# Kernel tuning notes

Measured on AMD Instinct MI355X. Metric: run time of the kernel, lower is better.

## Reference

```python
import jax, jax.numpy as jnp
import numpy as np

N_EXPERTS = 8
TOP_K = 2


def setup_inputs() -> dict:
    key = jax.random.key(0)
    k1, k2, k3, k4 = jax.random.split(key, 4)
    B, S, D, E = 8, 4096, 1024, N_EXPERTS
    x = jax.random.normal(k1, (B, S, D), dtype=jnp.float32)
    gate_w = jax.random.normal(k2, (D, E), dtype=jnp.float32) * (1.0 / np.sqrt(D))
    expert_w = jax.random.normal(k3, (E, D, D), dtype=jnp.float32) * (1.0 / np.sqrt(D))
    expert_b = jax.random.normal(k4, (E, D), dtype=jnp.float32) * 0.01
    return {"x": x, "gate_w": gate_w, "expert_w": expert_w, "expert_b": expert_b}


def reference(x, gate_w, expert_w, expert_b):
    B, S, D = x.shape
    E = expert_w.shape[0]
    xt = x.reshape(-1, D)                       # [T, D], T = B*S
    T = xt.shape[0]
    gate_logits = xt @ gate_w                   # [T, E]
    weights, selected = jax.lax.top_k(gate_logits, TOP_K)   # [T, K]
    weights = jax.nn.softmax(weights.astype(jnp.float32), axis=1).astype(x.dtype)
    # Per-token combine weights over experts (top-k indices are distinct -> scatter-add is exact)
    combine = jnp.zeros((T, E), dtype=x.dtype).at[jnp.arange(T)[:, None], selected].add(weights)  # [T, E]
    out = jnp.zeros_like(xt)
    for e in range(E):  # fixed small expert count, mirrors the module's expert loop
        out = out + combine[:, e:e + 1] * (xt @ expert_w[e] + expert_b[e])
    return out.reshape(x.shape)
```

## Files before the change

### kernel.cpp

```cpp
#include <hip/hip_runtime.h>
#include <hip/hip_bf16.h>


typedef __attribute__((ext_vector_type(8))) short short8_t;
typedef __attribute__((ext_vector_type(4))) float f32x4_t;

#define GLOAD_LDS16(g, l)                                                                     \
  __builtin_amdgcn_global_load_lds((const __attribute__((address_space(1))) unsigned int*)(g), \
                                   (__attribute__((address_space(3))) unsigned int*)(l), 16, 0, 0)

__device__ __forceinline__ unsigned short f2bf(float f) {
  union { __hip_bfloat16 h; unsigned short u; } c;
  c.h = __float2bfloat16(f);
  return c.u;
}

__global__ __launch_bounds__(256) void gate_kernel(
    const float* __restrict__ x, const float* __restrict__ gw,
    unsigned short* __restrict__ xb,
    int* __restrict__ tok_e, float* __restrict__ tok_w)
{
  int wid = threadIdx.x >> 6, lane = threadIdx.x & 63;
  int t0 = (blockIdx.x << 4) + (wid << 2);
  const float4* g4 = (const float4*)gw;
  float lg[4][8] = {};
  #pragma unroll
  for (int c = 0; c < 4; ++c) {
    int d4 = (c << 6) + lane;
    float4 ga[4], gb[4];
    #pragma unroll
    for (int j = 0; j < 4; ++j) {
      int d = (d4 << 2) + j;
      ga[j] = g4[d << 1];
      gb[j] = g4[(d << 1) + 1];
    }
    #pragma unroll
    for (int t = 0; t < 4; ++t) {
      const float4* x4 = (const float4*)(x + ((size_t)(t0 + t) << 10));
      float4 v = x4[d4];
      unsigned long long pk = (unsigned long long)f2bf(v.x)
                            | ((unsigned long long)f2bf(v.y) << 16)
                            | ((unsigned long long)f2bf(v.z) << 32)
                            | ((unsigned long long)f2bf(v.w) << 48);
      ((unsigned long long*)(xb + ((size_t)(t0 + t) << 10)))[d4] = pk;
      float xs[4] = {v.x, v.y, v.z, v.w};
      #pragma unroll
      for (int j = 0; j < 4; ++j) {
        lg[t][0] += xs[j]*ga[j].x; lg[t][1] += xs[j]*ga[j].y;
        lg[t][2] += xs[j]*ga[j].z; lg[t][3] += xs[j]*ga[j].w;
        lg[t][4] += xs[j]*gb[j].x; lg[t][5] += xs[j]*gb[j].y;
        lg[t][6] += xs[j]*gb[j].z; lg[t][7] += xs[j]*gb[j].w;
      }
    }
  }
  #pragma unroll
  for (int t = 0; t < 4; ++t)
    #pragma unroll
    for (int e = 0; e < 8; ++e) {
      float v = lg[t][e];
      #pragma unroll
      for (int s = 32; s > 0; s >>= 1) v += __shfl_xor(v, s, 64);
      lg[t][e] = v;
    }
  if (lane < 4) {
    int t = t0 + lane;
    float m0 = lg[lane][0], m1 = -3.4e38f; int e0 = 0, e1 = 0;
    #pragma unroll
    for (int e = 1; e < 8; ++e) {
      float v = lg[lane][e];
      if (v > m0) { m1 = m0; e1 = e0; m0 = v; e0 = e; }
      else if (v > m1) { m1 = v; e1 = e; }
    }
    float p1 = 1.0f / (1.0f + expf(m0 - m1));
    float p0 = 1.0f - p1;
    int i0 = t << 1;
    tok_e[i0]   = e0; tok_w[i0]   = p0;
    tok_e[i0+1] = e1; tok_w[i0+1] = p1;
  }
}

__global__ __launch_bounds__(256) void hist_kernel(
    const int* __restrict__ tok_e, int* __restrict__ tok_r, int* __restrict__ chunkhist)
{
  __shared__ int lh[8];
  if (threadIdx.x < 8) lh[threadIdx.x] = 0;
  __syncthreads();
  int i = (blockIdx.x << 8) + threadIdx.x;
  int e = tok_e[i];
  tok_r[i] = atomicAdd(&lh[e], 1);
  __syncthreads();
  if (threadIdx.x < 8) chunkhist[(blockIdx.x << 3) + threadIdx.x] = lh[threadIdx.x];
}

__global__ __launch_bounds__(512) void scan_kernel(
    const int* __restrict__ chunkhist, int* __restrict__ base, int* __restrict__ ctrl)
{
  __shared__ int h[2048];
  __shared__ int bx[2048];
  __shared__ int tot[8], eoff[8];
  for (int i = threadIdx.x; i < 2048; i += 512) h[i] = chunkhist[i];
  __syncthreads();
  int wid = threadIdx.x >> 6, lane = threadIdx.x & 63;
  int running = 0;
  #pragma unroll
  for (int b = 0; b < 4; ++b) {
    int c = (b << 6) + lane;
    int orig = h[(c << 3) + wid];
    int v = orig;
    #pragma unroll
    for (int s = 1; s < 64; s <<= 1) {
      int u = __shfl_up(v, s, 64);
      if (lane >= s) v += u;
    }
    bx[(c << 3) + wid] = running + v - orig;
    running += __shfl(v, 63, 64);
  }
  if (lane == 0) tot[wid] = running;
  __syncthreads();
  if (threadIdx.x == 0) {
    int off = 0, boff = 0;
    #pragma unroll
    for (int e = 0; e < 8; ++e) {
      ctrl[e] = tot[e];
      ctrl[8 + e] = off; eoff[e] = off; off += tot[e];
      ctrl[16 + e] = boff; boff += (tot[e] + 255) >> 8;
    }
    ctrl[24] = boff;
  }
  __syncthreads();
  for (int i = threadIdx.x; i < 2048; i += 512) base[i] = bx[i] + eoff[i & 7];
}

__global__ __launch_bounds__(256) void scatter_kernel(
    const int* __restrict__ tok_e, const int* __restrict__ tok_r, const float* __restrict__ tok_w,
    const int* __restrict__ base, int* __restrict__ slot_token, float* __restrict__ slot_w,
    int* __restrict__ tok_slot)
{
  int i = (blockIdx.x << 8) + threadIdx.x;
  int e = tok_e[i];
  int slot = base[((i >> 8) << 3) + e] + tok_r[i];
  slot_token[slot] = i >> 1;
  slot_w[slot] = tok_w[i];
  tok_slot[i] = slot;
}

__global__ __launch_bounds__(256) void wconv_kernel(const float* __restrict__ w,
                                                    unsigned short* __restrict__ wt)
{
  __shared__ float tile[32][33];
  const float* we = w + ((size_t)blockIdx.z << 20);
  unsigned short* wte = wt + ((size_t)blockIdx.z << 20);
  int k0 = blockIdx.x << 5, n0 = blockIdx.y << 5;
  for (int i = threadIdx.x; i < 1024; i += 256) {
    int k = i >> 5, n = i & 31;
    tile[k][n] = we[(size_t)(k0 + k) * 1024 + n0 + n];
  }
  __syncthreads();
  for (int i = threadIdx.x; i < 1024; i += 256) {
    int n = i >> 5, k = i & 31;
    wte[(size_t)(n0 + n) * 1024 + k0 + k] = f2bf(tile[k][n]);
  }
}

__global__ __launch_bounds__(512, 2) void moe_gemm(
    const unsigned short* __restrict__ xb, const unsigned short* __restrict__ wt,
    const float* __restrict__ bias, const int* __restrict__ ctrl,
    const int* __restrict__ slot_token, const float* __restrict__ slot_w,
    float* __restrict__ ybuf, float* __restrict__ out, int total_slots, int use_ybuf)
{
  __shared__ unsigned short Alds[2 * 256 * 64];
  __shared__ unsigned short Blds[2 * 256 * 64];
  __shared__ int   tokid[256];
  __shared__ float wrow[256];

  int d = blockIdx.x;
  int xcd = d & 7, nb = (d >> 3) & 3, gbase = d >> 5;
  int by = (gbase << 3) | xcd;
  if (by >= ctrl[24]) return;
  int e = 0;
  #pragma unroll
  for (int i = 1; i < 8; ++i) if (by >= ctrl[16 + i]) e = i;
  int mblk = by - ctrl[16 + e];
  int cnt  = ctrl[e];
  int slot0 = ctrl[8 + e] + (mblk << 8);
  int rows_valid = cnt - (mblk << 8); if (rows_valid > 256) rows_valid = 256;

  int tid = threadIdx.x;
  if (tid < 256) {
    int s = slot0 + tid; if (s > total_slots - 1) s = total_slots - 1;
    tokid[tid] = slot_token[s];
    wrow[tid]  = slot_w[s];
  }
  __syncthreads();

  int lane = tid & 63, w = tid >> 6;
  int wm = w >> 2, wn = w & 3;
  int l15 = lane & 15, hk = lane >> 4;
  int bn0 = nb << 8;
  const unsigned short* wte = wt + ((size_t)e << 20);

  int rsub = tid >> 3;
  int kswz = (tid & 7) ^ (rsub & 7);
  const unsigned short* As[4];
  const unsigned short* Bs[4];
  #pragma unroll
  for (int j = 0; j < 4; ++j) {
    As[j] = xb  + ((size_t)tokid[(j << 6) + rsub] << 10) + (kswz << 3);
    Bs[j] = wte + ((size_t)(bn0 + (j << 6) + rsub) << 10) + (kswz << 3);
  }

  f32x4_t acc[8][4] = {};
  short8_t aN[4][2], aF1[4][2], bF0[2][2], bF1[2][2];

#define LDSA(base, ar, kk) (*(const short8_t*)&Alds[(base) + ((ar) << 6) + (((((kk) << 2) + hk) ^ ((ar) & 7)) << 3)])
#define LDSB(base, br, kk) (*(const short8_t*)&Blds[(base) + ((br) << 6) + (((((kk) << 2) + hk) ^ ((br) & 7)) << 3)])
#define QUAD(AF, BF, MB, NB)                                                            \
  _Pragma("unroll") for (int mf = 0; mf < 4; ++mf)                                      \
  _Pragma("unroll") for (int nf = 0; nf < 2; ++nf)                                      \
  _Pragma("unroll") for (int kk = 0; kk < 2; ++kk)                                      \
    acc[(MB)*4+mf][(NB)*2+nf] = __builtin_amdgcn_mfma_f32_16x16x32_bf16(                \
        AF[mf][kk], BF[nf][kk], acc[(MB)*4+mf][(NB)*2+nf], 0, 0, 0);

  #pragma unroll
  for (int j = 0; j < 4; ++j) GLOAD_LDS16(As[j], &Alds[(j << 12) + (w << 9)]);
  #pragma unroll
  for (int j = 0; j < 4; ++j) GLOAD_LDS16(Bs[j], &Blds[(j << 12) + (w << 9)]);
  asm volatile("s_waitcnt vmcnt(4)" ::: "memory");
  __builtin_amdgcn_s_barrier();
  #pragma unroll
  for (int mf = 0; mf < 4; ++mf)
    #pragma unroll
    for (int kk = 0; kk < 2; ++kk)
      aN[mf][kk] = LDSA(0, (wm << 7) + (mf << 4) + l15, kk);

  int tb = 0;
  for (int t = 0; t < 15; ++t) {
    int ntb = tb ^ 16384;
    int koff = (t + 1) << 6;
    #pragma unroll
    for (int j = 0; j < 4; ++j)
      GLOAD_LDS16(As[j] + koff, &Alds[ntb + (j << 12) + (w << 9)]);
    asm volatile("s_waitcnt vmcnt(4)" ::: "memory");
    __builtin_amdgcn_s_barrier();
    #pragma unroll
    for (int nf = 0; nf < 2; ++nf)
      #pragma unroll
      for (int kk = 0; kk < 2; ++kk)
        bF0[nf][kk] = LDSB(tb, (wn << 6) + (nf << 4) + l15, kk);
    __builtin_amdgcn_s_setprio(1);
    QUAD(aN, bF0, 0, 0)
    __builtin_amdgcn_s_setprio(0);
    #pragma unroll
    for (int j = 0; j < 4; ++j)
      GLOAD_LDS16(Bs[j] + koff, &Blds[ntb + (j << 12) + (w << 9)]);
    __builtin_amdgcn_s_barrier();
    #pragma unroll
    for (int nf = 0; nf < 2; ++nf)
      #pragma unroll
      for (int kk = 0; kk < 2; ++kk)
        bF1[nf][kk] = LDSB(tb, (wn << 6) + ((nf + 2) << 4) + l15, kk);
    __builtin_amdgcn_s_setprio(1);
    QUAD(aN, bF1, 0, 1)
    __builtin_amdgcn_s_setprio(0);
    __builtin_amdgcn_s_barrier();
    #pragma unroll
    for (int mf = 0; mf < 4; ++mf)
      #pragma unroll
      for (int kk = 0; kk < 2; ++kk)
        aF1[mf][kk] = LDSA(tb, (wm << 7) + 64 + (mf << 4) + l15, kk);
    __builtin_amdgcn_s_setprio(1);
    QUAD(aF1, bF1, 1, 1)
    __builtin_amdgcn_s_setprio(0);
    asm volatile("s_waitcnt vmcnt(4)" ::: "memory");
    __builtin_amdgcn_s_barrier();
    #pragma unroll
    for (int mf = 0; mf < 4; ++mf)
      #pragma unroll
      for (int kk = 0; kk < 2; ++kk)
        aN[mf][kk] = LDSA(ntb, (wm << 7) + (mf << 4) + l15, kk);
    __builtin_amdgcn_s_setprio(1);
    QUAD(aF1, bF0, 1, 0)
    __builtin_amdgcn_s_setprio(0);
    tb = ntb;
  }
  asm volatile("s_waitcnt vmcnt(0)" ::: "memory");
  __builtin_amdgcn_s_barrier();
  #pragma unroll
  for (int nf = 0; nf < 2; ++nf)
    #pragma unroll
    for (int kk = 0; kk < 2; ++kk) {
      bF0[nf][kk] = LDSB(tb, (wn << 6) + (nf << 4) + l15, kk);
      bF1[nf][kk] = LDSB(tb, (wn << 6) + ((nf + 2) << 4) + l15, kk);
    }
  #pragma unroll
  for (int mf = 0; mf < 4; ++mf)
    #pragma unroll
    for (int kk = 0; kk < 2; ++kk)
      aF1[mf][kk] = LDSA(tb, (wm << 7) + 64 + (mf << 4) + l15, kk);
  __builtin_amdgcn_s_setprio(1);
  QUAD(aN, bF0, 0, 0)
  QUAD(aN, bF1, 0, 1)
  QUAD(aF1, bF1, 1, 1)
  QUAD(aF1, bF0, 1, 0)
  __builtin_amdgcn_s_setprio(0);
#undef LDSA
#undef LDSB
#undef QUAD

  const float* be = bias + (e << 10);
  float bv[4];
  #pragma unroll
  for (int nf = 0; nf < 4; ++nf) bv[nf] = be[bn0 + (wn << 6) + (nf << 4) + l15];
  #pragma unroll
  for (int mf = 0; mf < 8; ++mf) {
    int rbase = (wm << 7) + (mf << 4) + (hk << 2);
    #pragma unroll
    for (int r = 0; r < 4; ++r) {
      int row = rbase + r;
      if (row < rows_valid) {
        float wv = wrow[row];
        if (use_ybuf) {
          size_t obase = ((size_t)(slot0 + row) << 10);
          #pragma unroll
          for (int nf = 0; nf < 4; ++nf) {
            int dout = bn0 + (wn << 6) + (nf << 4) + l15;
            ybuf[obase + dout] = wv * (acc[mf][nf][r] + bv[nf]);
          }
        } else {
          size_t obase = ((size_t)tokid[row] << 10);
          #pragma unroll
          for (int nf = 0; nf < 4; ++nf) {
            int dout = bn0 + (wn << 6) + (nf << 4) + l15;
            atomicAdd(&out[obase + dout], wv * (acc[mf][nf][r] + bv[nf]));
          }
        }
      }
    }
  }
}

__global__ __launch_bounds__(256) void combine_kernel(
    const float* __restrict__ ybuf, const int* __restrict__ tok_slot, float* __restrict__ out)
{
  int t = blockIdx.x;
  int s0 = tok_slot[t << 1], s1 = tok_slot[(t << 1) + 1];
  const float4* y0 = (const float4*)(ybuf + ((size_t)s0 << 10));
  const float4* y1 = (const float4*)(ybuf + ((size_t)s1 << 10));
  float4 a = y0[threadIdx.x], b = y1[threadIdx.x];
  float4 r; r.x = a.x + b.x; r.y = a.y + b.y; r.z = a.z + b.z; r.w = a.w + b.w;
  ((float4*)(out + ((size_t)t << 10)))[threadIdx.x] = r;
}

extern "C" void kernel_launch(void* const* d_in, const int* in_sizes, int n_in,
                              void* d_out, int out_size, void* d_ws, size_t ws_size,
                              hipStream_t stream) {
  (void)n_in;
  const float* x  = (const float*)d_in[0];
  const float* gw = (const float*)d_in[1];
  const float* ew = (const float*)d_in[2];
  const float* eb = (const float*)d_in[3];
  int T  = in_sizes[0] >> 10;
  int T2 = T << 1;

  char* wsb = (char*)d_ws;
  unsigned short* xb = (unsigned short*)wsb;
  size_t off = (size_t)T * 1024 * 2;
  unsigned short* wt = (unsigned short*)(wsb + off);
  off += (size_t)8 * 1024 * 1024 * 2;
  int* ctrl = (int*)(wsb + off); off += 256;
  int* tok_e = (int*)(wsb + off); off += (size_t)T2 * 4;
  int* tok_r = (int*)(wsb + off); off += (size_t)T2 * 4;
  float* tok_w = (float*)(wsb + off); off += (size_t)T2 * 4;
  int* slot_token = (int*)(wsb + off); off += (size_t)T2 * 4;
  float* slot_w = (float*)(wsb + off); off += (size_t)T2 * 4;
  int* tok_slot = (int*)(wsb + off); off += (size_t)T2 * 4;
  int* chunkhist = (int*)(wsb + off); off += 2048 * 4;
  int* base = (int*)(wsb + off); off += 2048 * 4;
  float* ybuf = (float*)(wsb + off);
  size_t need = off + (size_t)T2 * 1024 * 4;
  int use_ybuf = (ws_size >= need) ? 1 : 0;

  float* out = (float*)d_out;

  if (!use_ybuf)
    hipMemsetAsync(d_out, 0, (size_t)out_size * sizeof(float), stream);
  gate_kernel<<<T / 16, 256, 0, stream>>>(x, gw, xb, tok_e, tok_w);
  wconv_kernel<<<dim3(32, 32, 8), 256, 0, stream>>>(ew, wt);
  hist_kernel<<<T2 / 256, 256, 0, stream>>>(tok_e, tok_r, chunkhist);
  scan_kernel<<<1, 512, 0, stream>>>(chunkhist, base, ctrl);
  scatter_kernel<<<T2 / 256, 256, 0, stream>>>(tok_e, tok_r, tok_w, base,
                                               slot_token, slot_w, tok_slot);
  moe_gemm<<<1056, 512, 0, stream>>>(xb, wt, eb, ctrl, slot_token, slot_w,
                                     ybuf, out, T2, use_ybuf);
  if (use_ybuf)
    combine_kernel<<<T, 256, 0, stream>>>(ybuf, tok_slot, out);
}
```

Baseline: 373.9 us.

## Prefetch A tiles two k-steps ahead and restructure the GEMM main-loop barrier schedule

The main loop of the expert GEMM kernel now issues A-tile global-to-LDS loads two iterations ahead, with an extra prologue load of the second A tile. B-tile loads move to the start of each iteration. Each LDS fragment read is fenced with sched_barrier and paired s_barriers so the compiler cannot interleave reads with MFMA clusters. The goal is to hide global latency for A and make the 8-wave ping-pong schedule more deterministic, at the cost of more barriers per iteration and tighter vmcnt accounting that could stall or race if the counts are wrong.

```diff
diff --git a/kernel.cpp b/kernel.cpp
--- a/kernel.cpp
+++ b/kernel.cpp
@@ -220,83 +220,77 @@
   _Pragma("unroll") for (int kk = 0; kk < 2; ++kk)                                      \
     acc[(MB)*4+mf][(NB)*2+nf] = __builtin_amdgcn_mfma_f32_16x16x32_bf16(                \
         AF[mf][kk], BF[nf][kk], acc[(MB)*4+mf][(NB)*2+nf], 0, 0, 0);
+#define RD_A(DST, base, mh)                                                             \
+  _Pragma("unroll") for (int mf = 0; mf < 4; ++mf)                                      \
+  _Pragma("unroll") for (int kk = 0; kk < 2; ++kk)                                      \
+    DST[mf][kk] = LDSA(base, (wm << 7) + ((mh) << 6) + (mf << 4) + l15, kk);
+#define RD_B(DST, base, nh)                                                             \
+  _Pragma("unroll") for (int nf = 0; nf < 2; ++nf)                                      \
+  _Pragma("unroll") for (int kk = 0; kk < 2; ++kk)                                      \
+    DST[nf][kk] = LDSB(base, (wn << 6) + ((nh) << 5) + (nf << 4) + l15, kk);
 
   #pragma unroll
   for (int j = 0; j < 4; ++j) GLOAD_LDS16(As[j], &Alds[(j << 12) + (w << 9)]);
   #pragma unroll
   for (int j = 0; j < 4; ++j) GLOAD_LDS16(Bs[j], &Blds[(j << 12) + (w << 9)]);
+  #pragma unroll
+  for (int j = 0; j < 4; ++j) GLOAD_LDS16(As[j] + 64, &Alds[16384 + (j << 12) + (w << 9)]);
   asm volatile("s_waitcnt vmcnt(4)" ::: "memory");
   __builtin_amdgcn_s_barrier();
-  #pragma unroll
-  for (int mf = 0; mf < 4; ++mf)
-    #pragma unroll
-    for (int kk = 0; kk < 2; ++kk)
-      aN[mf][kk] = LDSA(0, (wm << 7) + (mf << 4) + l15, kk);
+  RD_A(aN, 0, 0)
 
   int tb = 0;
   for (int t = 0; t < 15; ++t) {
     int ntb = tb ^ 16384;
-    int koff = (t + 1) << 6;
-    #pragma unroll
-    for (int j = 0; j < 4; ++j)
-      GLOAD_LDS16(As[j] + koff, &Alds[ntb + (j << 12) + (w << 9)]);
-    asm volatile("s_waitcnt vmcnt(4)" ::: "memory");
-    __builtin_amdgcn_s_barrier();
-    #pragma unroll
-    for (int nf = 0; nf < 2; ++nf)
+    {
+      int koffB = (t + 1) << 6;
       #pragma unroll
-      for (int kk = 0; kk < 2; ++kk)
-        bF0[nf][kk] = LDSB(tb, (wn << 6) + (nf << 4) + l15, kk);
+      for (int j = 0; j < 4; ++j)
+        GLOAD_LDS16(Bs[j] + koffB, &Blds[ntb + (j << 12) + (w << 9)]);
+    }
+    RD_B(bF0, tb, 0)
+    __builtin_amdgcn_sched_barrier(0);
+    __builtin_amdgcn_s_barrier();
     __builtin_amdgcn_s_setprio(1);
     QUAD(aN, bF0, 0, 0)
     __builtin_amdgcn_s_setprio(0);
-    #pragma unroll
-    for (int j = 0; j < 4; ++j)
-      GLOAD_LDS16(Bs[j] + koff, &Blds[ntb + (j << 12) + (w << 9)]);
-    __builtin_amdgcn_s_barrier();
-    #pragma unroll
-    for (int nf = 0; nf < 2; ++nf)
-      #pragma unroll
-      for (int kk = 0; kk < 2; ++kk)
-        bF1[nf][kk] = LDSB(tb, (wn << 6) + ((nf + 2) << 4) + l15, kk);
+    __builtin_amdgcn_s_barrier();
+    RD_B(bF1, tb, 1)
+    __builtin_amdgcn_sched_barrier(0);
+    __builtin_amdgcn_s_barrier();
     __builtin_amdgcn_s_setprio(1);
     QUAD(aN, bF1, 0, 1)
     __builtin_amdgcn_s_setprio(0);
     __builtin_amdgcn_s_barrier();
-    #pragma unroll
-    for (int mf = 0; mf < 4; ++mf)
-      #pragma unroll
-      for (int kk = 0; kk < 2; ++kk)
-        aF1[mf][kk] = LDSA(tb, (wm << 7) + 64 + (mf << 4) + l15, kk);
+    RD_A(aF1, tb, 1)
+    asm volatile("s_waitcnt vmcnt(4)" ::: "memory");
+    __builtin_amdgcn_sched_barrier(0);
+    __builtin_amdgcn_s_barrier();
     __builtin_amdgcn_s_setprio(1);
     QUAD(aF1, bF1, 1, 1)
     __builtin_amdgcn_s_setprio(0);
+    __builtin_amdgcn_s_barrier();
+    if (t < 14) {
+      int koffA = (t + 2) << 6;
+      #pragma unroll
+      for (int j = 0; j < 4; ++j)
+        GLOAD_LDS16(As[j] + koffA, &Alds[tb + (j << 12) + (w << 9)]);
+    }
     asm volatile("s_waitcnt vmcnt(4)" ::: "memory");
-    __builtin_amdgcn_s_barrier();
-    #pragma unroll
-    for (int mf = 0; mf < 4; ++mf)
-      #pragma unroll
-      for (int kk = 0; kk < 2; ++kk)
-        aN[mf][kk] = LDSA(ntb, (wm << 7) + (mf << 4) + l15, kk);
+    RD_A(aN, ntb, 0)
+    __builtin_amdgcn_sched_barrier(0);
+    __builtin_amdgcn_s_barrier();
     __builtin_amdgcn_s_setprio(1);
     QUAD(aF1, bF0, 1, 0)
     __builtin_amdgcn_s_setprio(0);
+    __builtin_amdgcn_s_barrier();
     tb = ntb;
   }
   asm volatile("s_waitcnt vmcnt(0)" ::: "memory");
   __builtin_amdgcn_s_barrier();
-  #pragma unroll
-  for (int nf = 0; nf < 2; ++nf)
-    #pragma unroll
-    for (int kk = 0; kk < 2; ++kk) {
-      bF0[nf][kk] = LDSB(tb, (wn << 6) + (nf << 4) + l15, kk);
-      bF1[nf][kk] = LDSB(tb, (wn << 6) + ((nf + 2) << 4) + l15, kk);
-    }
-  #pragma unroll
-  for (int mf = 0; mf < 4; ++mf)
-    #pragma unroll
-    for (int kk = 0; kk < 2; ++kk)
-      aF1[mf][kk] = LDSA(tb, (wm << 7) + 64 + (mf << 4) + l15, kk);
+  RD_B(bF0, tb, 0)
+  RD_B(bF1, tb, 1)
+  RD_A(aF1, tb, 1)
   __builtin_amdgcn_s_setprio(1);
   QUAD(aN, bF0, 0, 0)
   QUAD(aN, bF1, 0, 1)
@@ -306,6 +300,8 @@
 #undef LDSA
 #undef LDSB
 #undef QUAD
+#undef RD_A
+#undef RD_B
 
   const float* be = bias + (e << 10);
   float bv[4];
```

Result: slower. 408.9 us (+9.4%).
